# Kernel tuning notes

Measured on AMD Instinct MI355X. Metric: run time of the kernel, lower is better.

The kernel has to match this reference:

```python
import jax, jax.numpy as jnp
import numpy as np
import math

D_MODEL = 768
D_INNER = 1536   # expand_factor=2
D_STATE = 16
DT_RANK = 48     # ceil(768/16)
D_CONV = 4
B, L = 2, 1024


def setup_inputs() -> dict:
    key = jax.random.key(0)
    ks = jax.random.split(key, 16)
    rn = lambda k, shape, s: jax.random.normal(k, shape, jnp.float32) * s
    dt_std = DT_RANK ** -0.5
    # dt bias init: softplus-inverse of dt in [dt_min, dt_max]
    dt = jnp.exp(jax.random.uniform(ks[6], (D_INNER,)) * (math.log(0.1) - math.log(0.001)) + math.log(0.001))
    dt = jnp.clip(dt, 1e-4, None)
    inv_dt = dt + jnp.log(-jnp.expm1(-dt))
    A_init = jnp.log(jnp.tile(jnp.arange(1, D_STATE + 1, dtype=jnp.float32), (D_INNER, 1)))
    return {
        "x": jax.random.normal(ks[0], (B, L, D_MODEL), jnp.float32),
        "in_proj_w": rn(ks[1], (2 * D_INNER, D_MODEL), D_MODEL ** -0.5),
        "conv_w": rn(ks[2], (D_INNER, D_CONV), D_CONV ** -0.5),
        "conv_bias": rn(ks[3], (D_INNER,), 0.02),
        "x_proj_w": rn(ks[4], (DT_RANK + 2 * D_STATE, D_INNER), D_INNER ** -0.5),
        "dt_proj_w": jax.random.uniform(ks[5], (D_INNER, DT_RANK), jnp.float32, -dt_std, dt_std),
        "dt_proj_b": inv_dt,
        "A_log": A_init,
        "D_param": jnp.ones((D_INNER,), jnp.float32),
        "out_proj_w": rn(ks[7], (D_MODEL, D_INNER), D_INNER ** -0.5),
        "A_b_log": A_init,
        "x_proj_b_w": rn(ks[8], (DT_RANK + 2 * D_STATE, D_INNER), D_INNER ** -0.5),
        "dt_proj_b_w": jax.random.uniform(ks[9], (D_INNER, DT_RANK), jnp.float32, -dt_std, dt_std),
        "dt_proj_b_b": inv_dt,
        "D_b": jnp.ones((D_INNER,), jnp.float32),
    }


def _ssm_dir(xs, A_log, Dv, xpw, dtw, dtb):
    # xs: [B, L, ED]
    A = -jnp.exp(A_log)                                  # [ED, N]
    dbc = xs @ xpw.T                                     # [B, L, dt_rank + 2N]
    delta = jax.nn.softplus(dbc[..., :DT_RANK] @ dtw.T + dtb)   # [B, L, ED]
    Bm = dbc[..., DT_RANK:DT_RANK + D_STATE]             # [B, L, N]
    Cm = dbc[..., DT_RANK + D_STATE:]                    # [B, L, N]
    dA = jnp.exp(delta[..., None] * A)                   # [B, L, ED, N]
    dBx = (delta * xs)[..., None] * Bm[:, :, None, :]    # [B, L, ED, N]

    def comb(e1, e2):
        a1, h1 = e1
        a2, h2 = e2
        return (a2 * a1, a2 * h1 + h2)

    _, hs = jax.lax.associative_scan(comb, (dA, dBx), axis=1)  # [B, L, ED, N]
    y = jnp.einsum('blen,bln->ble', hs, Cm)
    return y + Dv * xs


def reference(x, in_proj_w, conv_w, conv_bias, x_proj_w, dt_proj_w, dt_proj_b,
              A_log, D_param, out_proj_w, A_b_log, x_proj_b_w, dt_proj_b_w,
              dt_proj_b_b, D_b):
    xz = x @ in_proj_w.T                                 # [B, L, 2*ED]
    xs, z = xz[..., :D_INNER], xz[..., D_INNER:]
    # causal depthwise conv1d (torch pads both sides then slices [:L] == left pad)
    xt = jnp.transpose(xs, (0, 2, 1))                    # [B, ED, L]
    conv = jax.lax.conv_general_dilated(
        xt, conv_w[:, None, :], (1,), [(D_CONV - 1, 0)],
        feature_group_count=D_INNER,
        dimension_numbers=('NCW', 'OIW', 'NCW'))
    xs = jax.nn.silu(jnp.transpose(conv + conv_bias[:, None], (0, 2, 1)))
    y = _ssm_dir(xs, A_log, D_param, x_proj_w, dt_proj_w, dt_proj_b)
    yb = _ssm_dir(xs[:, ::-1], A_b_log, D_b, x_proj_b_w, dt_proj_b_w, dt_proj_b_b)
    y = y + yb[:, ::-1]
    return (y * jax.nn.silu(z)) @ out_proj_w.T
```

## Files before the change

kernel.cpp:

```cpp
#include <hip/hip_runtime.h>
#include <hip/hip_bf16.h>
#include <math.h>
#include <stdint.h>

#define D_MODEL 768
#define D_INNER 1536
#define D_STATE 16
#define DT_RANK 48
#define NB 2
#define LL 1024
#define MROWS (NB*LL)
#define NXZ (2*D_INNER)
#define NDBC 80

typedef __attribute__((ext_vector_type(8))) short short8;
typedef __attribute__((ext_vector_type(4))) float f32x4;

__device__ __forceinline__ float silu_f(float x) {
  return x / (1.0f + __expf(-x));
}
__device__ __forceinline__ float softplus_f(float x) {
  return (x >= 20.0f) ? x : log1pf(__expf(x));
}

__device__ __forceinline__ ushort f2bf(float x) {
  union { float f; uint32_t u; } v; v.f = x;
  return (ushort)((v.u + 0x7FFFu + ((v.u >> 16) & 1u)) >> 16);
}
__device__ __forceinline__ float bf2f(ushort h) {
  union { uint32_t u; float f; } v; v.u = ((uint32_t)h) << 16;
  return v.f;
}

__device__ __forceinline__ void g2l16(const void* g, void* l) {
  __builtin_amdgcn_global_load_lds(
      (const __attribute__((address_space(1))) uint32_t*)g,
      (__attribute__((address_space(3))) uint32_t*)l, 16, 0, 0);
}

__device__ __forceinline__ int swz(int row) {
  return (row ^ (row >> 2)) & 3;
}

__global__ __launch_bounds__(256)
void cvt_split_kernel(const float* __restrict__ in, ushort* __restrict__ hi,
                      ushort* __restrict__ lo, int n4) {
  int i = blockIdx.x * 256 + threadIdx.x;
  if (i >= n4) return;
  float4 v = *(const float4*)&in[i*4];
  ushort4 h, l;
  h.x = f2bf(v.x); l.x = f2bf(v.x - bf2f(h.x));
  h.y = f2bf(v.y); l.y = f2bf(v.y - bf2f(h.y));
  h.z = f2bf(v.z); l.z = f2bf(v.z - bf2f(h.z));
  h.w = f2bf(v.w); l.w = f2bf(v.w - bf2f(h.w));
  *(ushort4*)&hi[i*4] = h;
  *(ushort4*)&lo[i*4] = l;
}

template<int BM, int BN>
__global__ __launch_bounds__(256)
void gemm_mfma(const ushort* __restrict__ Ah, const ushort* __restrict__ Al,
               const ushort* __restrict__ Bh, const ushort* __restrict__ Bl,
               float* __restrict__ C, int M, int N, int K) {
  constexpr int MR = BM / 32;
  constexpr int NR = BN / 32;
  __shared__ __align__(16) ushort sAh[BM*32];
  __shared__ __align__(16) ushort sAl[BM*32];
  __shared__ __align__(16) ushort sBh[BN*32];
  __shared__ __align__(16) ushort sBl[BN*32];

  const int tid  = threadIdx.x;
  const int w    = tid >> 6;
  const int lane = tid & 63;
  const int wr   = w >> 1, wc = w & 1;
  const int bm   = blockIdx.x * BM, bn = blockIdx.y * BN;

  const int rA = lane >> 2;
  const int ps = lane & 3;
  const int kg = lane >> 4;
  const int fr = lane & 15;

  f32x4 acc[MR][NR];
  #pragma unroll
  for (int mi = 0; mi < MR; ++mi)
    #pragma unroll
    for (int ni = 0; ni < NR; ++ni) acc[mi][ni] = (f32x4){0.f,0.f,0.f,0.f};

  for (int k0 = 0; k0 < K; k0 += 32) {
    __syncthreads();
    #pragma unroll
    for (int q = 0; q < BM/64; ++q) {
      int row = q*64 + w*16 + rA;
      int kch = ps ^ swz(row);
      size_t go = (size_t)(bm + row)*K + k0 + kch*8;
      g2l16(Ah + go, (ushort*)sAh + (q*64 + w*16)*32);
      g2l16(Al + go, (ushort*)sAl + (q*64 + w*16)*32);
    }
    #pragma unroll
    for (int q = 0; q < BN/64; ++q) {
      int row = q*64 + w*16 + rA;
      int kch = ps ^ swz(row);
      size_t go = (size_t)(bn + row)*K + k0 + kch*8;
      g2l16(Bh + go, (ushort*)sBh + (q*64 + w*16)*32);
      g2l16(Bl + go, (ushort*)sBl + (q*64 + w*16)*32);
    }
    __syncthreads();

    short8 ah[MR], al[MR], bh[NR], bl[NR];
    #pragma unroll
    for (int mi = 0; mi < MR; ++mi) {
      int row  = wr*(BM/2) + mi*16 + fr;
      int slot = kg ^ swz(row);
      ah[mi] = *(const short8*)((const char*)sAh + row*64 + slot*16);
      al[mi] = *(const short8*)((const char*)sAl + row*64 + slot*16);
    }
    #pragma unroll
    for (int ni = 0; ni < NR; ++ni) {
      int row  = wc*(BN/2) + ni*16 + fr;
      int slot = kg ^ swz(row);
      bh[ni] = *(const short8*)((const char*)sBh + row*64 + slot*16);
      bl[ni] = *(const short8*)((const char*)sBl + row*64 + slot*16);
    }
    #pragma unroll
    for (int mi = 0; mi < MR; ++mi)
      #pragma unroll
      for (int ni = 0; ni < NR; ++ni) {
        acc[mi][ni] = __builtin_amdgcn_mfma_f32_16x16x32_bf16(ah[mi], bh[ni], acc[mi][ni], 0, 0, 0);
        acc[mi][ni] = __builtin_amdgcn_mfma_f32_16x16x32_bf16(ah[mi], bl[ni], acc[mi][ni], 0, 0, 0);
        acc[mi][ni] = __builtin_amdgcn_mfma_f32_16x16x32_bf16(al[mi], bh[ni], acc[mi][ni], 0, 0, 0);
      }
  }

  #pragma unroll
  for (int mi = 0; mi < MR; ++mi)
    #pragma unroll
    for (int ni = 0; ni < NR; ++ni) {
      #pragma unroll
      for (int r = 0; r < 4; ++r) {
        int m = bm + wr*(BM/2) + mi*16 + kg*4 + r;
        int n = bn + wc*(BN/2) + ni*16 + fr;
        C[(size_t)m*N + n] = acc[mi][ni][r];
      }
    }
}

__global__ __launch_bounds__(256)
void conv_silu_kernel(const float* __restrict__ xz, const float* __restrict__ cw,
                      const float* __restrict__ cb, float* __restrict__ xsc) {
  int idx = blockIdx.x * 256 + threadIdx.x;
  if (idx >= MROWS * D_INNER) return;
  int e   = idx % D_INNER;
  int row = idx / D_INNER;
  int l   = row % LL;
  const float* base = xz + (size_t)row * NXZ + e;
  float s = cb[e];
  #pragma unroll
  for (int j = 0; j < 4; ++j) {
    int dl = j - 3;
    if (l + dl >= 0) {
      int off = dl * NXZ;
      s = fmaf(cw[e*4 + j], base[off], s);
    }
  }
  xsc[idx] = silu_f(s);
}

__global__ __launch_bounds__(256)
void zero_kernel(float* __restrict__ p, int n) {
  int i = blockIdx.x * 256 + threadIdx.x;
  if (i < n) p[i] = 0.0f;
}

#define XP_BM 16
#define XP_KC 192
__global__ __launch_bounds__(256)
void xproj_kernel(const float* __restrict__ xsc, const float* __restrict__ wf,
                  const float* __restrict__ wb, float* __restrict__ dbcf,
                  float* __restrict__ dbcb) {
  __shared__ __align__(16) float As[16][XP_BM];
  __shared__ __align__(16) float Ws[16][164];
  const int m0    = blockIdx.x * XP_BM;
  const int kbase = blockIdx.y * XP_KC;
  const int tid = threadIdx.x;
  const int tx = tid & 31;
  const int ty = tid >> 5;
  float acc[2][5] = {};
  for (int k0 = kbase; k0 < kbase + XP_KC; k0 += 16) {
    __syncthreads();
    if (tid < 64) {
      int r = tid >> 2, c = (tid & 3) * 4;
      float4 v = *(const float4*)&xsc[(size_t)(m0 + r)*D_INNER + k0 + c];
      As[c+0][r] = v.x; As[c+1][r] = v.y; As[c+2][r] = v.z; As[c+3][r] = v.w;
    }
    for (int q = tid; q < 640; q += 256) {
      int r = q >> 2, c = (q & 3) * 4;
      const float* src = (r < 80) ? &wf[(size_t)r*D_INNER + k0 + c]
                                  : &wb[(size_t)(r-80)*D_INNER + k0 + c];
      float4 v = *(const float4*)src;
      Ws[c+0][r] = v.x; Ws[c+1][r] = v.y; Ws[c+2][r] = v.z; Ws[c+3][r] = v.w;
    }
    __syncthreads();
    #pragma unroll
    for (int kk = 0; kk < 16; ++kk) {
      float a0 = As[kk][ty*2 + 0];
      float a1 = As[kk][ty*2 + 1];
      #pragma unroll
      for (int j = 0; j < 5; ++j) {
        float w = Ws[kk][tx*5 + j];
        acc[0][j] = fmaf(a0, w, acc[0][j]);
        acc[1][j] = fmaf(a1, w, acc[1][j]);
      }
    }
  }
  #pragma unroll
  for (int i = 0; i < 2; ++i) {
    int m = m0 + ty*2 + i;
    #pragma unroll
    for (int j = 0; j < 5; ++j) {
      int n = tx*5 + j;
      float v = acc[i][j];
      if (n < 80) atomicAdd(&dbcf[(size_t)m*NDBC + n], v);
      else        atomicAdd(&dbcb[(size_t)m*NDBC + (n-80)], v);
    }
  }
}

__global__ __launch_bounds__(256)
void delta_kernel(const float* __restrict__ dbcf, const float* __restrict__ dbcb,
                  const float* __restrict__ dtwf, const float* __restrict__ dtwb,
                  const float* __restrict__ dtbf, const float* __restrict__ dtbb,
                  float* __restrict__ outf, float* __restrict__ outb) {
  const int dir = blockIdx.z;
  const float* dbc = dir ? dbcb : dbcf;
  const float* dtw = dir ? dtwb : dtwf;
  const float* dtb = dir ? dtbb : dtbf;
  float* out = dir ? outb : outf;
  __shared__ __align__(16) float As[48][36];
  __shared__ __align__(16) float Ws[48][132];
  const int m0 = blockIdx.x * 32;
  const int e0 = blockIdx.y * 128;
  const int tid = threadIdx.x;
  const int tx = tid & 31;
  const int ty = tid >> 5;
  for (int q = tid; q < 384; q += 256) {
    int r = q / 12, c = (q % 12) * 4;
    float4 v = *(const float4*)&dbc[(size_t)(m0 + r)*NDBC + c];
    As[c+0][r] = v.x; As[c+1][r] = v.y; As[c+2][r] = v.z; As[c+3][r] = v.w;
  }
  for (int q = tid; q < 1536; q += 256) {
    int r = q / 12, c = (q % 12) * 4;
    float4 v = *(const float4*)&dtw[(size_t)(e0 + r)*DT_RANK + c];
    Ws[c+0][r] = v.x; Ws[c+1][r] = v.y; Ws[c+2][r] = v.z; Ws[c+3][r] = v.w;
  }
  __syncthreads();
  float acc[4][4] = {};
  #pragma unroll
  for (int kk = 0; kk < 48; ++kk) {
    float4 a = *(const float4*)&As[kk][ty*4];
    float4 w = *(const float4*)&Ws[kk][tx*4];
    float av[4] = {a.x, a.y, a.z, a.w};
    float wv[4] = {w.x, w.y, w.z, w.w};
    #pragma unroll
    for (int i = 0; i < 4; ++i)
      #pragma unroll
      for (int j = 0; j < 4; ++j)
        acc[i][j] = fmaf(av[i], wv[j], acc[i][j]);
  }
  #pragma unroll
  for (int i = 0; i < 4; ++i) {
    int m = m0 + ty*4 + i;
    float4 o;
    o.x = softplus_f(acc[i][0] + dtb[e0 + tx*4 + 0]);
    o.y = softplus_f(acc[i][1] + dtb[e0 + tx*4 + 1]);
    o.z = softplus_f(acc[i][2] + dtb[e0 + tx*4 + 2]);
    o.w = softplus_f(acc[i][3] + dtb[e0 + tx*4 + 3]);
    *(float4*)&out[(size_t)m*D_INNER + e0 + tx*4] = o;
  }
}

#define SC_C 16
#define SC_P 64
__global__ __launch_bounds__(1024)
void scan_kernel(const float* __restrict__ deltaf, const float* __restrict__ deltab,
                 const float* __restrict__ dbcf, const float* __restrict__ dbcb,
                 const float* __restrict__ xsc,
                 const float* __restrict__ Alogf, const float* __restrict__ Alogb,
                 float* __restrict__ yf, float* __restrict__ yb) {
  __shared__ float sA[SC_C][4][16];
  __shared__ float sH[SC_C][4][16];
  __shared__ float sI[SC_C][4][16];
  const int blk = blockIdx.x;
  const int dir = blk / 768;
  const int b   = (blk % 768) / 384;
  const int e0  = (blk % 384) * 4;
  const int tid = threadIdx.x;
  const int c   = tid >> 6;
  const int lane = tid & 63;
  const int es  = lane >> 4;
  const int n   = lane & 15;
  const int e   = e0 + es;

  const float* delta = dir ? deltab : deltaf;
  const float* dbc   = dir ? dbcb  : dbcf;
  const float* Alog  = dir ? Alogb : Alogf;
  float* y           = dir ? yb    : yf;

  const float a = -__expf(Alog[e*D_STATE + n]);
  const float* dp = delta + (size_t)b * LL * D_INNER + e;
  const float* xp = xsc   + (size_t)b * LL * D_INNER + e;
  const float* cp = dbc   + (size_t)b * LL * NDBC;
  float*       yp = y     + (size_t)b * LL * D_INNER + e;

  float Ap = 1.0f, hh = 0.0f;
  #pragma unroll 4
  for (int i = 0; i < SC_P; ++i) {
    const int tau = c * SC_P + i;
    const int l = dir ? (LL - 1 - tau) : tau;
    const float dl = dp[(size_t)l * D_INNER];
    const float xv = xp[(size_t)l * D_INNER];
    const float Bv = cp[l*NDBC + DT_RANK + n];
    const float dA = __expf(dl * a);
    hh = fmaf(dA, hh, dl * xv * Bv);
    Ap *= dA;
  }
  sA[c][es][n] = Ap;
  sH[c][es][n] = hh;
  __syncthreads();

  if (tid < 64) {
    float carry = 0.0f;
    #pragma unroll
    for (int cc = 0; cc < SC_C; ++cc) {
      sI[cc][es][n] = carry;
      carry = fmaf(sA[cc][es][n], carry, sH[cc][es][n]);
    }
  }
  __syncthreads();

  float h = sI[c][es][n];
  #pragma unroll 4
  for (int i = 0; i < SC_P; ++i) {
    const int tau = c * SC_P + i;
    const int l = dir ? (LL - 1 - tau) : tau;
    const float dl = dp[(size_t)l * D_INNER];
    const float xv = xp[(size_t)l * D_INNER];
    const float Bv = cp[l*NDBC + DT_RANK + n];
    const float Cv = cp[l*NDBC + DT_RANK + D_STATE + n];
    const float dA = __expf(dl * a);
    h = fmaf(dA, h, dl * xv * Bv);
    float p = h * Cv;
    p += __shfl_xor(p, 1);
    p += __shfl_xor(p, 2);
    p += __shfl_xor(p, 4);
    p += __shfl_xor(p, 8);
    if (n == 0) yp[(size_t)l * D_INNER] = p;
  }
}

__global__ __launch_bounds__(256)
void gate_kernel(const float* __restrict__ yf, const float* __restrict__ yb,
                 const float* __restrict__ xsc, const float* __restrict__ xz,
                 const float* __restrict__ Dp, const float* __restrict__ Db,
                 ushort* __restrict__ ghi, ushort* __restrict__ glo) {
  int i4 = blockIdx.x * 256 + threadIdx.x;
  if (i4 >= MROWS * D_INNER / 4) return;
  int idx = i4 * 4;
  int e   = idx % D_INNER;
  int row = idx / D_INNER;
  float4 vf = *(const float4*)&yf[idx];
  float4 vb = *(const float4*)&yb[idx];
  float4 vx = *(const float4*)&xsc[idx];
  float4 vz = *(const float4*)&xz[(size_t)row*NXZ + D_INNER + e];
  float4 vD  = *(const float4*)&Dp[e];
  float4 vDb = *(const float4*)&Db[e];
  float4 o;
  o.x = fmaf(vD.x + vDb.x, vx.x, vf.x + vb.x) * silu_f(vz.x);
  o.y = fmaf(vD.y + vDb.y, vx.y, vf.y + vb.y) * silu_f(vz.y);
  o.z = fmaf(vD.z + vDb.z, vx.z, vf.z + vb.z) * silu_f(vz.z);
  o.w = fmaf(vD.w + vDb.w, vx.w, vf.w + vb.w) * silu_f(vz.w);
  ushort4 h, l;
  h.x = f2bf(o.x); l.x = f2bf(o.x - bf2f(h.x));
  h.y = f2bf(o.y); l.y = f2bf(o.y - bf2f(h.y));
  h.z = f2bf(o.z); l.z = f2bf(o.z - bf2f(h.z));
  h.w = f2bf(o.w); l.w = f2bf(o.w - bf2f(h.w));
  *(ushort4*)&ghi[idx] = h;
  *(ushort4*)&glo[idx] = l;
}

extern "C" void kernel_launch(void* const* d_in, const int* in_sizes, int n_in,
                              void* d_out, int out_size, void* d_ws, size_t ws_size,
                              hipStream_t stream) {
  const float* x     = (const float*)d_in[0];
  const float* ipw   = (const float*)d_in[1];
  const float* cw    = (const float*)d_in[2];
  const float* cb    = (const float*)d_in[3];
  const float* xpwf  = (const float*)d_in[4];
  const float* dtwf  = (const float*)d_in[5];
  const float* dtbf  = (const float*)d_in[6];
  const float* Alogf = (const float*)d_in[7];
  const float* Dpf   = (const float*)d_in[8];
  const float* opw   = (const float*)d_in[9];
  const float* Alogb = (const float*)d_in[10];
  const float* xpwb  = (const float*)d_in[11];
  const float* dtwb  = (const float*)d_in[12];
  const float* dtbb  = (const float*)d_in[13];
  const float* Dpb   = (const float*)d_in[14];
  float* out = (float*)d_out;

  float* ws = (float*)d_ws;
  float* xz   = ws;
  float* xsc  = xz   + (size_t)MROWS * NXZ;
  float* dbcf = xsc  + (size_t)MROWS * D_INNER;
  float* dbcb = dbcf + (size_t)MROWS * NDBC;
  float* dltf = dbcb + (size_t)MROWS * NDBC;
  float* dltb = dltf + (size_t)MROWS * D_INNER;
  float* yfb  = dltb + (size_t)MROWS * D_INNER;
  float* ybb  = yfb  + (size_t)MROWS * D_INNER;
  ushort* xhi   = (ushort*)yfb;
  ushort* xlo   = xhi   + (size_t)MROWS * D_MODEL;
  ushort* ipwhi = (ushort*)ybb;
  ushort* ipwlo = ipwhi + (size_t)NXZ * D_MODEL;
  ushort* opwhi = (ushort*)(ybb + (size_t)MROWS * D_INNER);
  ushort* opwlo = opwhi + (size_t)D_MODEL * D_INNER;
  ushort* ghi = (ushort*)dltf;
  ushort* glo = ghi + (size_t)MROWS * D_INNER;

  cvt_split_kernel<<<dim3(MROWS*D_MODEL/4/256), 256, 0, stream>>>(x, xhi, xlo, MROWS*D_MODEL/4);
  cvt_split_kernel<<<dim3(NXZ*D_MODEL/4/256), 256, 0, stream>>>(ipw, ipwhi, ipwlo, NXZ*D_MODEL/4);
  cvt_split_kernel<<<dim3(D_MODEL*D_INNER/4/256), 256, 0, stream>>>(opw, opwhi, opwlo, D_MODEL*D_INNER/4);

  gemm_mfma<128,128><<<dim3(MROWS/128, NXZ/128), 256, 0, stream>>>(
      xhi, xlo, ipwhi, ipwlo, xz, MROWS, NXZ, D_MODEL);
  conv_silu_kernel<<<dim3((MROWS*D_INNER)/256), 256, 0, stream>>>(xz, cw, cb, xsc);
  zero_kernel<<<dim3((MROWS*2*NDBC + 255)/256), 256, 0, stream>>>(dbcf, MROWS*2*NDBC);
  xproj_kernel<<<dim3(MROWS/XP_BM, D_INNER/XP_KC), 256, 0, stream>>>(
      xsc, xpwf, xpwb, dbcf, dbcb);
  delta_kernel<<<dim3(MROWS/32, D_INNER/128, 2), 256, 0, stream>>>(
      dbcf, dbcb, dtwf, dtwb, dtbf, dtbb, dltf, dltb);
  scan_kernel<<<dim3(1536), 1024, 0, stream>>>(
      dltf, dltb, dbcf, dbcb, xsc, Alogf, Alogb, yfb, ybb);
  gate_kernel<<<dim3((MROWS*D_INNER/4)/256), 256, 0, stream>>>(
      yfb, ybb, xsc, xz, Dpf, Dpb, ghi, glo);
  gemm_mfma<128,64><<<dim3(MROWS/128, D_MODEL/64), 256, 0, stream>>>(
      ghi, glo, opwhi, opwlo, out, MROWS, D_MODEL, D_INNER);
}
```

Before: 507.9 us.

## Store delta and conv output channel-major so scan reads contiguous along L

Delta kernel now writes delta transposed ([E][M]) through a shared-memory staging tile, and a new transpose kernel produces a channel-major copy of the conv/SiLU output, so the scan kernel reads delta and x contiguously along the sequence for each channel. This is meant to replace strided per-timestep loads of 1536-float stride with sequential accesses. It adds a transpose pass, extra workspace, and shared-memory staging in the delta kernel. Separately, the output projection GEMM tile is reduced from 128x64 to 64x64 to launch more blocks.

```diff
diff --git a/kernel.cpp b/kernel.cpp
--- a/kernel.cpp
+++ b/kernel.cpp
@@ -163,6 +163,24 @@
     }
   }
   xsc[idx] = silu_f(s);
+}
+
+__global__ __launch_bounds__(256)
+void transpose_kernel(const float* __restrict__ in, float* __restrict__ outT) {
+  __shared__ float T[64][65];
+  const int m0 = blockIdx.x * 64;
+  const int e0 = blockIdx.y * 64;
+  const int cr = threadIdx.x >> 4;
+  const int cc = (threadIdx.x & 15) * 4;
+  for (int rr = cr; rr < 64; rr += 16) {
+    float4 v = *(const float4*)&in[(size_t)(m0 + rr)*D_INNER + e0 + cc];
+    T[rr][cc+0] = v.x; T[rr][cc+1] = v.y; T[rr][cc+2] = v.z; T[rr][cc+3] = v.w;
+  }
+  __syncthreads();
+  for (int er = cr; er < 64; er += 16) {
+    float4 v = make_float4(T[cc+0][er], T[cc+1][er], T[cc+2][er], T[cc+3][er]);
+    *(float4*)&outT[(size_t)(e0 + er)*MROWS + m0 + cc] = v;
+  }
 }
 
 __global__ __launch_bounds__(256)
@@ -237,6 +255,7 @@
   float* out = dir ? outb : outf;
   __shared__ __align__(16) float As[48][36];
   __shared__ __align__(16) float Ws[48][132];
+  __shared__ float T[128][33];
   const int m0 = blockIdx.x * 32;
   const int e0 = blockIdx.y * 128;
   const int tid = threadIdx.x;
@@ -267,23 +286,28 @@
         acc[i][j] = fmaf(av[i], wv[j], acc[i][j]);
   }
   #pragma unroll
-  for (int i = 0; i < 4; ++i) {
-    int m = m0 + ty*4 + i;
-    float4 o;
-    o.x = softplus_f(acc[i][0] + dtb[e0 + tx*4 + 0]);
-    o.y = softplus_f(acc[i][1] + dtb[e0 + tx*4 + 1]);
-    o.z = softplus_f(acc[i][2] + dtb[e0 + tx*4 + 2]);
-    o.w = softplus_f(acc[i][3] + dtb[e0 + tx*4 + 3]);
-    *(float4*)&out[(size_t)m*D_INNER + e0 + tx*4] = o;
+  for (int i = 0; i < 4; ++i)
+    #pragma unroll
+    for (int j = 0; j < 4; ++j)
+      T[tx*4 + j][ty*4 + i] = softplus_f(acc[i][j] + dtb[e0 + tx*4 + j]);
+  __syncthreads();
+  {
+    int r = tid >> 1, h = (tid & 1) * 16;
+    float* dst = out + (size_t)(e0 + r)*MROWS + m0 + h;
+    #pragma unroll
+    for (int q = 0; q < 4; ++q) {
+      float4 v = make_float4(T[r][h+q*4+0], T[r][h+q*4+1], T[r][h+q*4+2], T[r][h+q*4+3]);
+      *(float4*)(dst + q*4) = v;
+    }
   }
 }
 
 #define SC_C 16
 #define SC_P 64
 __global__ __launch_bounds__(1024)
-void scan_kernel(const float* __restrict__ deltaf, const float* __restrict__ deltab,
+void scan_kernel(const float* __restrict__ dltf, const float* __restrict__ dltb,
                  const float* __restrict__ dbcf, const float* __restrict__ dbcb,
-                 const float* __restrict__ xsc,
+                 const float* __restrict__ xst,
                  const float* __restrict__ Alogf, const float* __restrict__ Alogb,
                  float* __restrict__ yf, float* __restrict__ yb) {
   __shared__ float sA[SC_C][4][16];
@@ -300,24 +324,24 @@
   const int n   = lane & 15;
   const int e   = e0 + es;
 
-  const float* delta = dir ? deltab : deltaf;
-  const float* dbc   = dir ? dbcb  : dbcf;
-  const float* Alog  = dir ? Alogb : Alogf;
-  float* y           = dir ? yb    : yf;
+  const float* dlt  = dir ? dltb  : dltf;
+  const float* dbc  = dir ? dbcb  : dbcf;
+  const float* Alog = dir ? Alogb : Alogf;
+  float* y          = dir ? yb    : yf;
 
   const float a = -__expf(Alog[e*D_STATE + n]);
-  const float* dp = delta + (size_t)b * LL * D_INNER + e;
-  const float* xp = xsc   + (size_t)b * LL * D_INNER + e;
-  const float* cp = dbc   + (size_t)b * LL * NDBC;
-  float*       yp = y     + (size_t)b * LL * D_INNER + e;
+  const float* dp = dlt + (size_t)e * MROWS + b * LL;
+  const float* xp = xst + (size_t)e * MROWS + b * LL;
+  const float* cp = dbc + (size_t)b * LL * NDBC;
+  float*       yp = y   + (size_t)b * LL * D_INNER + e;
 
   float Ap = 1.0f, hh = 0.0f;
   #pragma unroll 4
   for (int i = 0; i < SC_P; ++i) {
     const int tau = c * SC_P + i;
     const int l = dir ? (LL - 1 - tau) : tau;
-    const float dl = dp[(size_t)l * D_INNER];
-    const float xv = xp[(size_t)l * D_INNER];
+    const float dl = dp[l];
+    const float xv = xp[l];
     const float Bv = cp[l*NDBC + DT_RANK + n];
     const float dA = __expf(dl * a);
     hh = fmaf(dA, hh, dl * xv * Bv);
@@ -342,8 +366,8 @@
   for (int i = 0; i < SC_P; ++i) {
     const int tau = c * SC_P + i;
     const int l = dir ? (LL - 1 - tau) : tau;
-    const float dl = dp[(size_t)l * D_INNER];
-    const float xv = xp[(size_t)l * D_INNER];
+    const float dl = dp[l];
+    const float xv = xp[l];
     const float Bv = cp[l*NDBC + DT_RANK + n];
     const float Cv = cp[l*NDBC + DT_RANK + D_STATE + n];
     const float dA = __expf(dl * a);
@@ -422,6 +446,7 @@
   ushort* ipwlo = ipwhi + (size_t)NXZ * D_MODEL;
   ushort* opwhi = (ushort*)(ybb + (size_t)MROWS * D_INNER);
   ushort* opwlo = opwhi + (size_t)D_MODEL * D_INNER;
+  float*  xst   = (float*)(opwlo + (size_t)D_MODEL * D_INNER);
   ushort* ghi = (ushort*)dltf;
   ushort* glo = ghi + (size_t)MROWS * D_INNER;
 
@@ -432,15 +457,16 @@
   gemm_mfma<128,128><<<dim3(MROWS/128, NXZ/128), 256, 0, stream>>>(
       xhi, xlo, ipwhi, ipwlo, xz, MROWS, NXZ, D_MODEL);
   conv_silu_kernel<<<dim3((MROWS*D_INNER)/256), 256, 0, stream>>>(xz, cw, cb, xsc);
+  transpose_kernel<<<dim3(MROWS/64, D_INNER/64), 256, 0, stream>>>(xsc, xst);
   zero_kernel<<<dim3((MROWS*2*NDBC + 255)/256), 256, 0, stream>>>(dbcf, MROWS*2*NDBC);
   xproj_kernel<<<dim3(MROWS/XP_BM, D_INNER/XP_KC), 256, 0, stream>>>(
       xsc, xpwf, xpwb, dbcf, dbcb);
   delta_kernel<<<dim3(MROWS/32, D_INNER/128, 2), 256, 0, stream>>>(
       dbcf, dbcb, dtwf, dtwb, dtbf, dtbb, dltf, dltb);
   scan_kernel<<<dim3(1536), 1024, 0, stream>>>(
-      dltf, dltb, dbcf, dbcb, xsc, Alogf, Alogb, yfb, ybb);
+      dltf, dltb, dbcf, dbcb, xst, Alogf, Alogb, yfb, ybb);
   gate_kernel<<<dim3((MROWS*D_INNER/4)/256), 256, 0, stream>>>(
       yfb, ybb, xsc, xz, Dpf, Dpb, ghi, glo);
-  gemm_mfma<128,64><<<dim3(MROWS/128, D_MODEL/64), 256, 0, stream>>>(
+  gemm_mfma<64,64><<<dim3(MROWS/64, D_MODEL/64), 256, 0, stream>>>(
       ghi, glo, opwhi, opwlo, out, MROWS, D_MODEL, D_INNER);
 }
```

Measured after the change: 482.0 us. 5.1% less time.
